# Kernel optimization log

Hardware: AMD Instinct MI355X
Metric: run time of the kernel (lower is better)

Reference implementation:

```python
import jax, jax.numpy as jnp
import numpy as np

PERCENTAGE = 0.26
BN_EPS = 1e-5


def _conv1x1(x, w, b):
    # x: (B,C,H,W), w: (O,C), b: (O,)
    return jnp.einsum('bchw,oc->bohw', x, w) + b[None, :, None, None]


def _bn_train(x, gamma, beta):
    # BatchNorm2d in training mode: biased variance over (B,H,W) per channel
    mean = x.mean(axis=(0, 2, 3), keepdims=True)
    var = jnp.mean((x - mean) ** 2, axis=(0, 2, 3), keepdims=True)
    xhat = (x - mean) * jax.lax.rsqrt(var + BN_EPS)
    return xhat * gamma[None, :, None, None] + beta[None, :, None, None]


def _band_mask(w, max_w):
    # The two mask-construction loops in the torch code reduce to |i-j| < max_w
    idx = jnp.arange(w)
    return jnp.abs(idx[:, None] - idx[None, :]) < max_w  # (w, w) bool


def setup_inputs() -> dict:
    key = jax.random.key(0)
    ks = jax.random.split(key, 16)
    B, C, H, W = 2, 256, 64, 512
    s = 0.02  # weight scale to keep attention logits in a sane range
    return {
        'x1': jax.random.normal(ks[0], (B, C, H, W), jnp.float32),
        'x2': jax.random.normal(ks[1], (B, C, H, W), jnp.float32),
        'Qw': jax.random.normal(ks[2], (C, C), jnp.float32) * s,
        'Qb': jax.random.normal(ks[3], (C,), jnp.float32) * s,
        'Kw': jax.random.normal(ks[4], (C, C), jnp.float32) * s,
        'Kb': jax.random.normal(ks[5], (C,), jnp.float32) * s,
        'Vw': jax.random.normal(ks[6], (C, C), jnp.float32) * s,
        'Vb': jax.random.normal(ks[7], (C,), jnp.float32) * s,
        'Vg': jax.random.normal(ks[8], (C,), jnp.float32),
        'Vbeta': jax.random.normal(ks[9], (C,), jnp.float32),
        'Ww': jax.random.normal(ks[10], (C, C), jnp.float32) * s,
        'Wb': jax.random.normal(ks[11], (C,), jnp.float32) * s,
        'Wg': jax.random.normal(ks[12], (C,), jnp.float32),
        'Wbeta': jax.random.normal(ks[13], (C,), jnp.float32),
    }


def reference(x1, x2, Qw, Qb, Kw, Kb, Vw, Vb, Vg, Vbeta, Ww, Wb, Wg, Wbeta):
    b, c, h, w = x1.shape
    max_w = int(w * PERCENTAGE)
    mask = _band_mask(w, max_w)  # (w, w), broadcasts over (b*h) rows
    neg_inf = jnp.float32(-jnp.inf)

    def rows(x):  # (B,C,H,W) -> (B*H, W, C)
        return x.transpose(0, 2, 3, 1).reshape(b * h, w, c)

    q1 = rows(_conv1x1(x1, Qw, Qb))
    q2 = rows(_conv1x1(x2, Qw, Qb))
    k1 = rows(_conv1x1(x1, Kw, Kb))  # (B*H, W, C); contract over C below
    k2 = rows(_conv1x1(x2, Kw, Kb))
    v1 = rows(_bn_train(_conv1x1(x1, Vw, Vb), Vg, Vbeta))
    v2 = rows(_bn_train(_conv1x1(x2, Vw, Vb), Vg, Vbeta))

    def attend(q, k, v):
        scores = jnp.einsum('nqc,nkc->nqk', q, k)  # (B*H, W, W)
        scores = jnp.where(mask[None], scores, neg_inf)
        p = jax.nn.softmax(scores, axis=-1)
        return jnp.einsum('nqk,nkc->nqc', p, v)

    def cols(y):  # (B*H, W, C) -> (B,C,H,W)
        return y.reshape(b, h, w, c).transpose(0, 3, 1, 2)

    y1 = cols(attend(q1, k2, v2))
    y2 = cols(attend(q2, k1, v1))
    z1 = _bn_train(_conv1x1(y1, Ww, Wb), Wg, Wbeta) + x1
    z2 = _bn_train(_conv1x1(y2, Ww, Wb), Wg, Wbeta) + x2
    return (z1, z2)
```

## Files before the change

### kernel.cpp

```cpp
#include <hip/hip_runtime.h>

typedef unsigned short u16;
typedef short bfrag __attribute__((ext_vector_type(8)));
typedef float ffrag __attribute__((ext_vector_type(4)));
typedef u16 u16x4 __attribute__((ext_vector_type(4)));
typedef float f4 __attribute__((ext_vector_type(4)));

#define MFMA16(a,b,c) __builtin_amdgcn_mfma_f32_16x16x32_bf16((a),(b),(c),0,0,0)

#define WAITV(N) do { asm volatile("s_waitcnt vmcnt(" #N ")" ::: "memory"); \
                      __builtin_amdgcn_sched_barrier(0); } while(0)
#define RBAR()   do { __builtin_amdgcn_s_barrier(); \
                      __builtin_amdgcn_sched_barrier(0); } while(0)


__device__ __forceinline__ u16 f2bf(float f){
  union { float f; unsigned int i; } cv; cv.f = f;
  unsigned int x = cv.i;
  return (u16)((x + 0x7fffu + ((x >> 16) & 1u)) >> 16);
}
__device__ __forceinline__ float bf2f(u16 u){
  union { unsigned int i; float f; } cv;
  cv.i = ((unsigned int)u) << 16;
  return cv.f;
}
__device__ __forceinline__ unsigned cvtpk(float lo, float hi){
  unsigned r; asm("v_cvt_pk_bf16_f32 %0, %1, %2" : "=v"(r) : "v"(lo), "v"(hi)); return r;
}
__device__ __forceinline__ bfrag ldb(const u16* p){
  bfrag v; __builtin_memcpy(&v, p, 16); return v;
}
__device__ __forceinline__ void gload_lds16(const u16* g, u16* l){
  __builtin_amdgcn_global_load_lds(
      (const __attribute__((address_space(1))) unsigned int*)g,
      (__attribute__((address_space(3))) unsigned int*)l, 16, 0, 0);
}

__global__ __launch_bounds__(256) void k_wcvt(const float* __restrict__ qw, const float* __restrict__ kw,
                                              const float* __restrict__ vw, const float* __restrict__ ww,
                                              u16* __restrict__ out){
  int t = blockIdx.x*256 + threadIdx.x;
  out[t]        = f2bf(qw[t]);
  out[t+65536]  = f2bf(kw[t]);
  out[t+131072] = f2bf(vw[t]);
  out[t+196608] = f2bf(ww[t]);
}

__global__ __launch_bounds__(256) void k_xpose(const float* __restrict__ x1, const float* __restrict__ x2,
                                               u16* __restrict__ xr1, u16* __restrict__ xr2){
  const float* x = blockIdx.z ? x2 : x1;
  u16* xr = blockIdx.z ? xr2 : xr1;
  __shared__ float T[64][65];
  int t = threadIdx.x;
  int p0 = blockIdx.x*64, c0 = blockIdx.y*64;
  int b = p0 >> 15, q0 = p0 & 32767;
  #pragma unroll
  for (int it=0; it<4; ++it){
    int cc = it*16 + (t>>4);
    int pi = (t&15)*4;
    ffrag v; __builtin_memcpy(&v, x + ((size_t)(b*256 + c0 + cc))*32768 + q0 + pi, 16);
    T[cc][pi+0]=v[0]; T[cc][pi+1]=v[1]; T[cc][pi+2]=v[2]; T[cc][pi+3]=v[3];
  }
  __syncthreads();
  int pi = t>>2, cj0 = (t&3)*16;
  u16 tmp[16];
  #pragma unroll
  for (int j=0;j<16;++j) tmp[j] = f2bf(T[cj0+j][pi]);
  __builtin_memcpy(xr + (size_t)(p0+pi)*256 + c0 + cj0, tmp, 32);
}

template<int NI>
__device__ __forceinline__ void stageT(const u16* __restrict__ src, int row0, int k0,
                                       u16* lds, int wid, int l){
  #pragma unroll
  for (int rr=0; rr<NI; ++rr){
    int off = rr*4096 + wid*1024 + l*16;
    int row = off>>7, inb = off&127;
    int srcb = inb ^ ((row&7)<<4);
    gload_lds16(src + (size_t)(row0+row)*256 + k0 + (srcb>>1),
                lds + ((rr*4096 + wid*1024)>>1));
  }
}

__global__ __launch_bounds__(256, 3) void k_qkv(const u16* __restrict__ xr1, const u16* __restrict__ xr2,
    const u16* __restrict__ wb,
    const float* __restrict__ qb, const float* __restrict__ kb, const float* __restrict__ vb,
    u16* __restrict__ Q1, u16* __restrict__ K1, u16* __restrict__ V1,
    u16* __restrict__ Q2, u16* __restrict__ K2, u16* __restrict__ V2){
  __shared__ __align__(16) u16 As[2][8192];
  __shared__ __align__(16) u16 Bs[2][4096];
  int id = blockIdx.x;
  int xcd = id & 7, j = id >> 3;
  int pl = j/24, v = j - pl*24;
  int ptile = xcd*64 + pl;
  int ot = v & 3, r = v >> 2;
  int wgt = r >> 1, s = r & 1;
  const u16* A = s ? xr2 : xr1;
  const u16* W = wb + wgt*65536;
  const float* bias = (wgt==0)? qb : (wgt==1)? kb : vb;

  int t = threadIdx.x, wid = t>>6, l = t&63, lr = l&15, lg = l>>4;
  int p0 = ptile*128, o0 = ot*64;
  int wr = wid*32;
  int swz = (lr&7)<<4;

  stageT<4>(A, p0, 0,  As[0], wid, l);
  stageT<2>(W, o0, 0,  Bs[0], wid, l);
  stageT<4>(A, p0, 64, As[1], wid, l);
  stageT<2>(W, o0, 64, Bs[1], wid, l);

  const ffrag fz = {0.f,0.f,0.f,0.f};
  ffrag acc[2][4];
  #pragma unroll
  for (int i=0;i<2;++i){ acc[i][0]=fz; acc[i][1]=fz; acc[i][2]=fz; acc[i][3]=fz; }

  #pragma unroll
  for (int ks=0; ks<4; ++ks){
    if (ks < 3) { WAITV(6); } else { WAITV(0); }
    RBAR();
    const u16* as = As[ks&1];
    const u16* bs = Bs[ks&1];
    #pragma unroll
    for (int kc=0; kc<2; ++kc){
      int colb = (kc*64 + lg*16) ^ swz;
      bfrag af[2], bf[4];
      #pragma unroll
      for (int mt=0; mt<2; ++mt)
        af[mt] = ldb(as + (((wr + mt*16 + lr)*128 + colb)>>1));
      #pragma unroll
      for (int nt=0; nt<4; ++nt)
        bf[nt] = ldb(bs + (((nt*16 + lr)*128 + colb)>>1));
      if (wgt != 2){
        #pragma unroll
        for (int mt=0; mt<2; ++mt)
          #pragma unroll
          for (int nt=0; nt<4; ++nt)
            acc[mt][nt] = MFMA16(bf[nt], af[mt], acc[mt][nt]);
      } else {
        #pragma unroll
        for (int mt=0; mt<2; ++mt)
          #pragma unroll
          for (int nt=0; nt<4; ++nt)
            acc[mt][nt] = MFMA16(af[mt], bf[nt], acc[mt][nt]);
      }
    }
    RBAR();
    if (ks < 2){
      stageT<4>(A, p0, (ks+2)*64, As[ks&1], wid, l);
      stageT<2>(W, o0, (ks+2)*64, Bs[ks&1], wid, l);
    }
  }

  if (wgt != 2){
    u16* op = (wgt==0) ? (s ? Q2 : Q1) : (s ? K2 : K1);
    #pragma unroll
    for (int nt=0; nt<4; ++nt){
      int ob = o0 + nt*16 + lg*4;
      ffrag bv = *reinterpret_cast<const ffrag*>(bias + ob);
      #pragma unroll
      for (int mt=0; mt<2; ++mt){
        int p = p0 + wr + mt*16 + lr;
        u16x4 vv;
        #pragma unroll
        for (int rr=0;rr<4;++rr) vv[rr] = f2bf(acc[mt][nt][rr] + bv[rr]);
        *reinterpret_cast<u16x4*>(op + (size_t)p*256 + ob) = vv;
      }
    }
  } else {
    u16* Vt = s ? V2 : V1;
    #pragma unroll
    for (int nt=0; nt<4; ++nt){
      int oo = o0 + nt*16 + lr;
      float bsc = bias[oo];
      #pragma unroll
      for (int mt=0; mt<2; ++mt){
        int pr = p0 + wr + mt*16 + lg*4;
        int n = pr >> 9, w0 = pr & 511;
        u16x4 vv;
        #pragma unroll
        for (int rr=0;rr<4;++rr) vv[rr] = f2bf(acc[mt][nt][rr] + bsc);
        *reinterpret_cast<u16x4*>(Vt + ((size_t)(n*256 + oo))*512 + w0) = vv;
      }
    }
  }
}

__global__ __launch_bounds__(256, 2) void k_conv1(const u16* __restrict__ in1, const u16* __restrict__ in2,
    const u16* __restrict__ wp, const float* __restrict__ bias,
    u16* __restrict__ o1, u16* __restrict__ o2,
    float* __restrict__ psum, float* __restrict__ psq){
  __shared__ __align__(16) u16 As[2][8192];
  __shared__ __align__(16) u16 Bs[2][8192];
  int id = blockIdx.x;
  int xcd = id & 7, j = id >> 3;
  int pl = j>>2, v = j&3;
  int ptile = xcd*64 + pl;
  int ot = v & 1, s = v >> 1;
  const u16* A = s ? in2 : in1;
  u16* out = s ? o2 : o1;

  int t = threadIdx.x, wid = t>>6, l = t&63, lr = l&15, lg = l>>4;
  int p0 = ptile*128, o0 = ot*128;
  int wr = (wid>>1)*64, wc = (wid&1)*64;
  int swz = (lr&7)<<4;

  stageT<4>(A, p0, 0,  As[0], wid, l);
  stageT<4>(wp, o0, 0, Bs[0], wid, l);
  stageT<4>(A, p0, 64, As[1], wid, l);
  stageT<4>(wp, o0, 64,Bs[1], wid, l);

  const ffrag fz = {0.f,0.f,0.f,0.f};
  ffrag acc[4][4];
  #pragma unroll
  for (int i=0;i<4;++i){ acc[i][0]=fz; acc[i][1]=fz; acc[i][2]=fz; acc[i][3]=fz; }

  #pragma unroll
  for (int ks=0; ks<4; ++ks){
    if (ks < 3) { WAITV(8); } else { WAITV(0); }
    RBAR();
    const u16* as = As[ks&1];
    const u16* bs = Bs[ks&1];
    #pragma unroll
    for (int kc=0; kc<2; ++kc){
      int colb = (kc*64 + lg*16) ^ swz;
      bfrag af[4], bfm[4];
      #pragma unroll
      for (int mt=0; mt<4; ++mt)
        af[mt] = ldb(as + (((wr + mt*16 + lr)*128 + colb)>>1));
      #pragma unroll
      for (int nt=0; nt<4; ++nt)
        bfm[nt] = ldb(bs + (((wc + nt*16 + lr)*128 + colb)>>1));
      #pragma unroll
      for (int mt=0; mt<4; ++mt)
        #pragma unroll
        for (int nt=0; nt<4; ++nt)
          acc[mt][nt] = MFMA16(af[mt], bfm[nt], acc[mt][nt]);
    }
    RBAR();
    if (ks < 2){
      stageT<4>(A, p0, (ks+2)*64, As[ks&1], wid, l);
      stageT<4>(wp, o0, (ks+2)*64, Bs[ks&1], wid, l);
    }
  }

  float pv[4], qv[4];
  #pragma unroll
  for (int nt=0; nt<4; ++nt){ pv[nt]=0.f; qv[nt]=0.f; }
  #pragma unroll
  for (int nt=0; nt<4; ++nt){
    int oo = o0 + wc + nt*16 + lr;
    float bsc = bias[oo];
    #pragma unroll
    for (int mt=0; mt<4; ++mt){
      int pr = p0 + wr + mt*16 + lg*4;
      #pragma unroll
      for (int rr=0;rr<4;++rr){
        float val = acc[mt][nt][rr] + bsc;
        out[(size_t)(pr + rr)*256 + oo] = f2bf(val);
        pv[nt] += val; qv[nt] += val*val;
      }
    }
  }
  #pragma unroll
  for (int nt=0; nt<4; ++nt){
    float sv = pv[nt], sq = qv[nt];
    sv += __shfl_xor(sv,16,64); sv += __shfl_xor(sv,32,64);
    sq += __shfl_xor(sq,16,64); sq += __shfl_xor(sq,32,64);
    if (lg==0){
      int oo = o0 + wc + nt*16 + lr;
      int idx = ((s*256 + oo)<<10) + (ptile<<1) + (wr>>6);
      psum[idx] = sv; psq[idx] = sq;
    }
  }
}

__global__ __launch_bounds__(256) void k_vstat1(const u16* __restrict__ V1, const u16* __restrict__ V2,
                                                float* __restrict__ ps, float* __restrict__ pq){
  int s = blockIdx.z;
  const u16* Vt = s ? V2 : V1;
  int c = blockIdx.x, ch = blockIdx.y, t = threadIdx.x;
  const u16* base = Vt + ((size_t)((ch*16 + (t>>4))*256 + c))*512 + (t&15)*32;
  float sm=0.f, sq=0.f;
  #pragma unroll
  for (int j=0;j<4;++j){
    bfrag v = ldb(base + j*8);
    #pragma unroll
    for (int e=0;e<8;++e){ float f = bf2f((u16)v[e]); sm+=f; sq+=f*f; }
  }
  __shared__ float rs[256], rq[256];
  rs[t]=sm; rq[t]=sq; __syncthreads();
  for (int st=128; st>0; st>>=1){ if (t<st){ rs[t]+=rs[t+st]; rq[t]+=rq[t+st]; } __syncthreads(); }
  if (t==0){ ps[s*2048 + c*8+ch]=rs[0]; pq[s*2048 + c*8+ch]=rq[0]; }
}
__global__ __launch_bounds__(256) void k_vstat2(const float* __restrict__ ps, const float* __restrict__ pq,
                                                const float* __restrict__ g, const float* __restrict__ be,
                                                float* __restrict__ aVall, float* __restrict__ bVall){
  int s = blockIdx.x, c = threadIdx.x;
  float sm=0.f, sq=0.f;
  #pragma unroll
  for (int ch=0; ch<8; ++ch){ sm += ps[s*2048 + c*8+ch]; sq += pq[s*2048 + c*8+ch]; }
  float mean = sm*(1.f/65536.f);
  float var  = sq*(1.f/65536.f) - mean*mean;
  float aa = g[c]*rsqrtf(var + 1e-5f);
  aVall[s*256+c]=aa; bVall[s*256+c]=be[c]-aa*mean;
}

__device__ __forceinline__ void stageK(const u16* Kn, u16* kb, int kt, int wid, int l){
  #pragma unroll
  for (int c2=0; c2<2; ++c2){
    int off = wid*2048 + c2*1024 + l*16;
    int row = off>>9, inb = off&511;
    int src = inb ^ ((row&7)<<4);
    gload_lds16(Kn + (size_t)(kt*16+row)*256 + (src>>1), kb + wid*1024 + c2*512);
  }
}
__device__ __forceinline__ void stageV(const u16* Vn, u16* vb, int k0, int wid, int l){
  #pragma unroll
  for (int c4=0; c4<4; ++c4){
    int off = wid*4096 + c4*1024 + l*16;
    int crow = off>>6, slot = (off>>4)&3;
    int kk = slot ^ ((crow>>1)&3);
    gload_lds16(Vn + (size_t)crow*512 + k0 + (kk<<3), vb + ((wid*4096 + c4*1024)>>1));
  }
}

__global__ __launch_bounds__(256, 2) void k_attn(
    const u16* __restrict__ Q1, const u16* __restrict__ K2, const u16* __restrict__ V2,
    const u16* __restrict__ Q2, const u16* __restrict__ K1, const u16* __restrict__ V1,
    const float* __restrict__ aVall, const float* __restrict__ bVall,
    u16* __restrict__ O1, u16* __restrict__ O2){
  __shared__ __align__(16) u16 KP[2][8192];
  __shared__ __align__(16) u16 VBs[2][8192];
  int t = threadIdx.x, wid = t>>6, l = t&63, lr = l&15, lg = l>>4;
  int id = blockIdx.x;
  int s = id >> 10;
  int r0 = id & 1023;
  int xcd = r0 & 7, s5 = r0 >> 3;
  int qb = s5 & 7, n = (xcd<<4) | (s5>>3);
  const u16* Q = s ? Q2 : Q1;
  const u16* K = s ? K1 : K2;
  const u16* V = s ? V1 : V2;
  const float* aV = aVall + (s ? 0 : 256);
  const float* bV = bVall + (s ? 0 : 256);
  u16* O = s ? O2 : O1;

  int q0 = qb*64, q0w = q0 + wid*16;
  int lo = q0 - 132; if (lo < 0) lo = 0;
  int hi = q0 + 195; if (hi > 511) hi = 511;
  int KTLO = (lo>>4) & ~1;
  int KTHI = (hi>>4) | 1;
  int nsteps = (KTHI - KTLO + 2) >> 1;

  const u16* Kn = K + (size_t)n*131072;
  const u16* Vn = V + (size_t)n*131072;

  bfrag qa[8];
  const u16* Qrow = Q + ((size_t)(n*512 + q0w + lr))*256 + lg*8;
  #pragma unroll
  for (int ks=0; ks<8; ++ks) qa[ks] = ldb(Qrow + ks*32);
  WAITV(0);

  stageK(Kn, KP[0],        KTLO+0, wid, l);
  stageK(Kn, KP[0]+4096,   KTLO+1, wid, l);
  stageV(Vn, VBs[0],       KTLO*16 + 0,  wid, l);
  stageK(Kn, KP[1],        KTLO+2, wid, l);
  stageK(Kn, KP[1]+4096,   KTLO+3, wid, l);
  stageV(Vn, VBs[1],       KTLO*16 + 32, wid, l);

  const ffrag fz = {0.f,0.f,0.f,0.f};
  ffrag o[16];
  #pragma unroll
  for (int i=0;i<16;++i) o[i] = fz;
  float lsum = 0.f;
  int q = q0w + lr;
  int s0l = lr + (lg&1)*32;
  bool hi2 = (lg & 2) != 0;
  int vswz = (lg ^ ((lr>>1)&3))<<3;

  #pragma unroll
  for (int sp=0; sp<12; ++sp){
    if (sp < nsteps){
      if (sp < nsteps-1) { WAITV(8); } else { WAITV(0); }
      RBAR();
      const u16* kp = KP[sp&1];
      const u16* vb = VBs[sp&1];

      ffrag sA = fz, sB = fz;
      #pragma unroll
      for (int ks=0; ks<8; ++ks){
        int boff = (ks*64 + lg*16) ^ ((lr&7)<<4);
        bfrag kfA = ldb(kp + ((lr*512 + boff)>>1));
        bfrag kfB = ldb(kp + 4096 + ((lr*512 + boff)>>1));
        sA = MFMA16(kfA, qa[ks], sA);
        sB = MFMA16(kfB, qa[ks], sB);
      }

      int baseA = q + 132 - ((KTLO + 2*sp)*16 + lg*4);
      #pragma unroll
      for (int r=0;r<4;++r){
        bool vA = (unsigned)(baseA - r)      < 265u;
        bool vB = (unsigned)(baseA - r - 16) < 265u;
        float eA = vA ? __expf(sA[r]) : 0.f;
        float eB = vB ? __expf(sB[r]) : 0.f;
        sA[r] = eA; sB[r] = eB; lsum += eA + eB;
      }

      unsigned pk0A = cvtpk(sA[0], sA[1]);
      unsigned pk1A = cvtpk(sA[2], sA[3]);
      unsigned pk0B = cvtpk(sB[0], sB[1]);
      unsigned pk1B = cvtpk(sB[2], sB[3]);
      unsigned a0 = (unsigned)__shfl((int)pk0A, s0l,    64);
      unsigned a1 = (unsigned)__shfl((int)pk1A, s0l,    64);
      unsigned a2 = (unsigned)__shfl((int)pk0A, s0l+16, 64);
      unsigned a3 = (unsigned)__shfl((int)pk1A, s0l+16, 64);
      unsigned b0 = (unsigned)__shfl((int)pk0B, s0l,    64);
      unsigned b1 = (unsigned)__shfl((int)pk1B, s0l,    64);
      unsigned b2 = (unsigned)__shfl((int)pk0B, s0l+16, 64);
      unsigned b3 = (unsigned)__shfl((int)pk1B, s0l+16, 64);
      unsigned pu[4];
      pu[0] = hi2 ? b0 : a0;  pu[1] = hi2 ? b1 : a1;
      pu[2] = hi2 ? b2 : a2;  pu[3] = hi2 ? b3 : a3;
      bfrag pa; __builtin_memcpy(&pa, pu, 16);

      #pragma unroll
      for (int ct=0; ct<16; ++ct){
        bfrag vf = ldb(vb + (ct*16 + lr)*32 + vswz);
        o[ct] = MFMA16(pa, vf, o[ct]);
      }
      RBAR();
      if (sp+2 < nsteps){
        stageK(Kn, KP[sp&1],      KTLO + 2*sp + 4, wid, l);
        stageK(Kn, KP[sp&1]+4096, KTLO + 2*sp + 5, wid, l);
        stageV(Vn, VBs[sp&1],     KTLO*16 + (sp+2)*32, wid, l);
      }
    }
  }

  lsum += __shfl_xor(lsum, 16, 64);
  lsum += __shfl_xor(lsum, 32, 64);
  float rinv = 1.f / lsum;
  float linv[4];
  #pragma unroll
  for (int r=0;r<4;++r) linv[r] = __shfl(rinv, (lg<<2)+r, 64);
  #pragma unroll
  for (int ct=0; ct<16; ++ct){
    int c = ct*16 + lr;
    float av = aV[c], bv = bV[c];
    #pragma unroll
    for (int r=0;r<4;++r)
      O[((size_t)(n*512 + q0w + lg*4 + r))*256 + c] = f2bf(av*(o[ct][r]*linv[r]) + bv);
  }
}

__global__ __launch_bounds__(256) void k_ustat2(const float* __restrict__ psum, const float* __restrict__ psq,
                                                const float* __restrict__ g, const float* __restrict__ be,
                                                float* __restrict__ aWall, float* __restrict__ bWall){
  int c = blockIdx.x, s = blockIdx.y, t = threadIdx.x;
  const float* ps = psum + (((size_t)s*256 + c)<<10);
  const float* pq = psq  + (((size_t)s*256 + c)<<10);
  float sm = ps[t] + ps[t+256] + ps[t+512] + ps[t+768];
  float sq = pq[t] + pq[t+256] + pq[t+512] + pq[t+768];
  __shared__ float rs[256], rq[256];
  rs[t]=sm; rq[t]=sq; __syncthreads();
  for (int st=128; st>0; st>>=1){ if (t<st){ rs[t]+=rs[t+st]; rq[t]+=rq[t+st]; } __syncthreads(); }
  if (t==0){
    float mean = rs[0]*(1.f/65536.f);
    float var  = rq[0]*(1.f/65536.f) - mean*mean;
    float aa = g[c]*rsqrtf(var + 1e-5f);
    aWall[s*256+c]=aa; bWall[s*256+c]=be[c]-aa*mean;
  }
}

__global__ __launch_bounds__(256) void k_final(const u16* __restrict__ u1, const u16* __restrict__ u2,
                                               const u16* __restrict__ xr1, const u16* __restrict__ xr2,
                                               const float* __restrict__ aWall, const float* __restrict__ bWall,
                                               float* __restrict__ z){
  int s = blockIdx.z;
  const u16* u  = s ? u2 : u1;
  const u16* xr = s ? xr2 : xr1;
  const float* aW = aWall + s*256;
  const float* bW = bWall + s*256;
  float* zb = z + (size_t)s*16777216;
  __shared__ u16 Tu[64][66], Tx[64][66];
  int t = threadIdx.x;
  int p0 = blockIdx.x*64, c0 = blockIdx.y*64;
  int b = p0>>15, q0 = p0&32767;
  #pragma unroll
  for (int it=0; it<4; ++it){
    int pi = it*16 + (t>>4);
    int cj = (t&15)*4;
    u16x4 vu; __builtin_memcpy(&vu, u  + (size_t)(p0+pi)*256 + c0 + cj, 8);
    u16x4 vx; __builtin_memcpy(&vx, xr + (size_t)(p0+pi)*256 + c0 + cj, 8);
    *reinterpret_cast<u16x4*>(&Tu[pi][cj]) = vu;
    *reinterpret_cast<u16x4*>(&Tx[pi][cj]) = vx;
  }
  __syncthreads();
  int qi4 = (t&15)*4;
  #pragma unroll
  for (int it=0; it<4; ++it){
    int cc = it*16 + (t>>4);
    float a = aW[c0+cc], bw = bW[c0+cc];
    f4 vz;
    #pragma unroll
    for (int j=0;j<4;++j)
      vz[j] = a*bf2f(Tu[qi4+j][cc]) + bw + bf2f(Tx[qi4+j][cc]);
    *reinterpret_cast<f4*>(zb + ((size_t)(b*256 + c0 + cc))*32768 + q0 + qi4) = vz;
  }
}

extern "C" void kernel_launch(void* const* d_in, const int* in_sizes, int n_in,
                              void* d_out, int out_size, void* d_ws, size_t ws_size,
                              hipStream_t stream) {
  const float* x1  = (const float*)d_in[0];
  const float* x2  = (const float*)d_in[1];
  const float* Qw  = (const float*)d_in[2];
  const float* Qb  = (const float*)d_in[3];
  const float* Kw  = (const float*)d_in[4];
  const float* Kb  = (const float*)d_in[5];
  const float* Vw  = (const float*)d_in[6];
  const float* Vb  = (const float*)d_in[7];
  const float* Vg  = (const float*)d_in[8];
  const float* Vbe = (const float*)d_in[9];
  const float* Ww  = (const float*)d_in[10];
  const float* Wb  = (const float*)d_in[11];
  const float* Wg  = (const float*)d_in[12];
  const float* Wbe = (const float*)d_in[13];

  char* ws = (char*)d_ws;
  const size_t S = 33554432;
  u16* xr1 = (u16*)(ws + 0*S);
  u16* xr2 = (u16*)(ws + 1*S);
  u16* Q1  = (u16*)(ws + 2*S);
  u16* K1  = (u16*)(ws + 3*S);
  u16* Q2  = (u16*)(ws + 4*S);
  u16* K2  = (u16*)(ws + 5*S);
  u16* wb  = (u16*)(ws + 6*S);
  float* vec = (float*)(ws + 6*S + 524288);
  float* aVall = vec;
  float* bVall = vec + 512;
  float* aWall = vec + 1024;
  float* bWall = vec + 1536;
  float* vps   = vec + 2048;
  float* vpq   = vps + 4096;

  char* douts = (char*)d_out;
  u16* Vt1 = (u16*)douts;
  u16* Vt2 = (u16*)(douts + S);
  u16* O1  = (u16*)(douts + 2*S);
  u16* O2  = (u16*)(douts + 3*S);
  float* upsum = (float*)douts;
  float* upsq  = upsum + 524288;
  u16* u1 = Q1;  u16* u2 = K1;
  float* z = (float*)d_out;

  dim3 gt(1024, 4, 2);
  dim3 gv(256, 8, 2);
  dim3 gu2(256, 2);

  k_wcvt<<<256, 256, 0, stream>>>(Qw, Kw, Vw, Ww, wb);
  k_xpose<<<gt, 256, 0, stream>>>(x1, x2, xr1, xr2);
  k_qkv<<<12288, 256, 0, stream>>>(xr1, xr2, wb, Qb, Kb, Vb, Q1, K1, Vt1, Q2, K2, Vt2);
  k_vstat1<<<gv, 256, 0, stream>>>(Vt1, Vt2, vps, vpq);
  k_vstat2<<<2, 256, 0, stream>>>(vps, vpq, Vg, Vbe, aVall, bVall);
  k_attn<<<2048, 256, 0, stream>>>(Q1, K2, Vt2, Q2, K1, Vt1, aVall, bVall, O1, O2);
  k_conv1<<<2048, 256, 0, stream>>>(O1, O2, wb + 196608, Wb, u1, u2, upsum, upsq);
  k_ustat2<<<gu2, 256, 0, stream>>>(upsum, upsq, Wg, Wbe, aWall, bWall);
  k_final<<<gt, 256, 0, stream>>>(u1, u2, xr1, xr2, aWall, bWall, z);
}
```

Measured before the change: 339.2 us.

## Fold Q and K projections into one merged weight and per-key bias term

Rewrites the attention scores as (x Qw^T Kw) x^T plus a per-key term, since the query bias and all key-bias contributions are constant along the softmax row except Qb·Kw·x_k. A merged weight Wq^T Wk is precomputed, the QKV GEMM now produces only XM and V, and attention reads the raw bf16 x as keys plus a precomputed per-key scalar c2 added before exp. This cuts a third of the projection GEMM work and the K writes, at the cost of extra small kernels, an extra bf16 rounding of the merged weight, and per-step c2 loads in the attention loop.

```diff
diff --git a/kernel.cpp b/kernel.cpp
--- a/kernel.cpp
+++ b/kernel.cpp
@@ -46,6 +46,47 @@
   out[t+196608] = f2bf(ww[t]);
 }
 
+__global__ __launch_bounds__(256) void k_g(const float* __restrict__ Qb, const u16* __restrict__ wb,
+                                           float* __restrict__ g){
+  int t = threadIdx.x;
+  float sm = 0.f;
+  #pragma unroll 8
+  for (int o=0;o<256;++o) sm += Qb[o]*bf2f(wb[65536 + o*256 + t]);
+  g[t] = sm;
+}
+
+__global__ __launch_bounds__(256) void k_mg(const u16* __restrict__ wb, u16* __restrict__ wm){
+  int c = blockIdx.x, t = threadIdx.x;
+  float sm = 0.f;
+  #pragma unroll 8
+  for (int o=0;o<256;++o) sm += bf2f(wb[o*256 + c]) * bf2f(wb[65536 + o*256 + t]);
+  wm[t*256 + c] = f2bf(sm);
+}
+
+__global__ __launch_bounds__(256) void k_c2(const u16* __restrict__ xr1, const u16* __restrict__ xr2,
+                                            const float* __restrict__ g, float* __restrict__ c2){
+  __shared__ float gs[256];
+  int t = threadIdx.x;
+  gs[t] = g[t];
+  __syncthreads();
+  int s = blockIdx.y;
+  const u16* xr = s ? xr2 : xr1;
+  float* out = c2 + s*65536;
+  int l = t & 63, w = t >> 6;
+  int half = l >> 5, cl = l & 31;
+  for (int it=0; it<16; ++it){
+    int row = blockIdx.x*128 + w*32 + it*2 + half;
+    bfrag v = ldb(xr + (size_t)row*256 + cl*8);
+    float sm = 0.f;
+    #pragma unroll
+    for (int e=0;e<8;++e) sm += bf2f((u16)v[e]) * gs[cl*8 + e];
+    sm += __shfl_xor(sm,1,64);  sm += __shfl_xor(sm,2,64);
+    sm += __shfl_xor(sm,4,64);  sm += __shfl_xor(sm,8,64);
+    sm += __shfl_xor(sm,16,64);
+    if (cl==0) out[row] = sm;
+  }
+}
+
 __global__ __launch_bounds__(256) void k_xpose(const float* __restrict__ x1, const float* __restrict__ x2,
                                                u16* __restrict__ xr1, u16* __restrict__ xr2){
   const float* x = blockIdx.z ? x2 : x1;
@@ -83,21 +124,20 @@
 }
 
 __global__ __launch_bounds__(256, 3) void k_qkv(const u16* __restrict__ xr1, const u16* __restrict__ xr2,
-    const u16* __restrict__ wb,
-    const float* __restrict__ qb, const float* __restrict__ kb, const float* __restrict__ vb,
-    u16* __restrict__ Q1, u16* __restrict__ K1, u16* __restrict__ V1,
-    u16* __restrict__ Q2, u16* __restrict__ K2, u16* __restrict__ V2){
+    const u16* __restrict__ wb, const u16* __restrict__ wm,
+    const float* __restrict__ vb,
+    u16* __restrict__ XM1, u16* __restrict__ V1,
+    u16* __restrict__ XM2, u16* __restrict__ V2){
   __shared__ __align__(16) u16 As[2][8192];
   __shared__ __align__(16) u16 Bs[2][4096];
   int id = blockIdx.x;
   int xcd = id & 7, j = id >> 3;
-  int pl = j/24, v = j - pl*24;
+  int pl = j >> 4, v = j & 15;
   int ptile = xcd*64 + pl;
   int ot = v & 3, r = v >> 2;
-  int wgt = r >> 1, s = r & 1;
+  int wgtV = r >> 1, s = r & 1;
   const u16* A = s ? xr2 : xr1;
-  const u16* W = wb + wgt*65536;
-  const float* bias = (wgt==0)? qb : (wgt==1)? kb : vb;
+  const u16* W = wgtV ? (wb + 131072) : wm;
 
   int t = threadIdx.x, wid = t>>6, l = t&63, lr = l&15, lg = l>>4;
   int p0 = ptile*128, o0 = ot*64;
@@ -130,7 +170,7 @@
       #pragma unroll
       for (int nt=0; nt<4; ++nt)
         bf[nt] = ldb(bs + (((nt*16 + lr)*128 + colb)>>1));
-      if (wgt != 2){
+      if (!wgtV){
         #pragma unroll
         for (int mt=0; mt<2; ++mt)
           #pragma unroll
@@ -151,18 +191,17 @@
     }
   }
 
-  if (wgt != 2){
-    u16* op = (wgt==0) ? (s ? Q2 : Q1) : (s ? K2 : K1);
+  if (!wgtV){
+    u16* op = s ? XM2 : XM1;
     #pragma unroll
     for (int nt=0; nt<4; ++nt){
       int ob = o0 + nt*16 + lg*4;
-      ffrag bv = *reinterpret_cast<const ffrag*>(bias + ob);
       #pragma unroll
       for (int mt=0; mt<2; ++mt){
         int p = p0 + wr + mt*16 + lr;
         u16x4 vv;
         #pragma unroll
-        for (int rr=0;rr<4;++rr) vv[rr] = f2bf(acc[mt][nt][rr] + bv[rr]);
+        for (int rr=0;rr<4;++rr) vv[rr] = f2bf(acc[mt][nt][rr]);
         *reinterpret_cast<u16x4*>(op + (size_t)p*256 + ob) = vv;
       }
     }
@@ -171,7 +210,7 @@
     #pragma unroll
     for (int nt=0; nt<4; ++nt){
       int oo = o0 + nt*16 + lr;
-      float bsc = bias[oo];
+      float bsc = vb[oo];
       #pragma unroll
       for (int mt=0; mt<2; ++mt){
         int pr = p0 + wr + mt*16 + lg*4;
@@ -325,9 +364,10 @@
 }
 
 __global__ __launch_bounds__(256, 2) void k_attn(
-    const u16* __restrict__ Q1, const u16* __restrict__ K2, const u16* __restrict__ V2,
-    const u16* __restrict__ Q2, const u16* __restrict__ K1, const u16* __restrict__ V1,
+    const u16* __restrict__ XM1, const u16* __restrict__ xr2, const u16* __restrict__ V2,
+    const u16* __restrict__ XM2, const u16* __restrict__ xr1, const u16* __restrict__ V1,
     const float* __restrict__ aVall, const float* __restrict__ bVall,
+    const float* __restrict__ c2all,
     u16* __restrict__ O1, u16* __restrict__ O2){
   __shared__ __align__(16) u16 KP[2][8192];
   __shared__ __align__(16) u16 VBs[2][8192];
@@ -337,11 +377,12 @@
   int r0 = id & 1023;
   int xcd = r0 & 7, s5 = r0 >> 3;
   int qb = s5 & 7, n = (xcd<<4) | (s5>>3);
-  const u16* Q = s ? Q2 : Q1;
-  const u16* K = s ? K1 : K2;
+  const u16* Q = s ? XM2 : XM1;
+  const u16* K = s ? xr1 : xr2;
   const u16* V = s ? V1 : V2;
   const float* aV = aVall + (s ? 0 : 256);
   const float* bV = bVall + (s ? 0 : 256);
+  const float* c2k = c2all + ((s^1)<<16) + n*512;
   u16* O = s ? O2 : O1;
 
   int q0 = qb*64, q0w = q0 + wid*16;
@@ -358,6 +399,13 @@
   const u16* Qrow = Q + ((size_t)(n*512 + q0w + lr))*256 + lg*8;
   #pragma unroll
   for (int ks=0; ks<8; ++ks) qa[ks] = ldb(Qrow + ks*32);
+  f4 c2A, c2B, c2An, c2Bn;
+  {
+    int colb0 = KTLO*16 + lg*4;
+    c2A = *reinterpret_cast<const f4*>(c2k + colb0);
+    c2B = *reinterpret_cast<const f4*>(c2k + colb0 + 16);
+    c2An = c2A; c2Bn = c2B;
+  }
   WAITV(0);
 
   stageK(Kn, KP[0],        KTLO+0, wid, l);
@@ -380,7 +428,9 @@
   #pragma unroll
   for (int sp=0; sp<12; ++sp){
     if (sp < nsteps){
-      if (sp < nsteps-1) { WAITV(8); } else { WAITV(0); }
+      if (sp == 0) { WAITV(8); }
+      else if (sp < nsteps-1) { WAITV(10); }
+      else { WAITV(0); }
       RBAR();
       const u16* kp = KP[sp&1];
       const u16* vb = VBs[sp&1];
@@ -400,8 +450,8 @@
       for (int r=0;r<4;++r){
         bool vA = (unsigned)(baseA - r)      < 265u;
         bool vB = (unsigned)(baseA - r - 16) < 265u;
-        float eA = vA ? __expf(sA[r]) : 0.f;
-        float eB = vB ? __expf(sB[r]) : 0.f;
+        float eA = vA ? __expf(sA[r] + c2A[r]) : 0.f;
+        float eB = vB ? __expf(sB[r] + c2B[r]) : 0.f;
         sA[r] = eA; sB[r] = eB; lsum += eA + eB;
       }
 
@@ -427,12 +477,19 @@
         bfrag vf = ldb(vb + (ct*16 + lr)*32 + vswz);
         o[ct] = MFMA16(pa, vf, o[ct]);
       }
+
+      if (sp+1 < nsteps){
+        int colbN = (KTLO + 2*(sp+1))*16 + lg*4;
+        c2An = *reinterpret_cast<const f4*>(c2k + colbN);
+        c2Bn = *reinterpret_cast<const f4*>(c2k + colbN + 16);
+      }
       RBAR();
       if (sp+2 < nsteps){
         stageK(Kn, KP[sp&1],      KTLO + 2*sp + 4, wid, l);
         stageK(Kn, KP[sp&1]+4096, KTLO + 2*sp + 5, wid, l);
         stageV(Vn, VBs[sp&1],     KTLO*16 + (sp+2)*32, wid, l);
       }
+      c2A = c2An; c2B = c2Bn;
     }
   }
 
@@ -525,15 +582,16 @@
   const float* Wb  = (const float*)d_in[11];
   const float* Wg  = (const float*)d_in[12];
   const float* Wbe = (const float*)d_in[13];
+  (void)Kb;
 
   char* ws = (char*)d_ws;
   const size_t S = 33554432;
   u16* xr1 = (u16*)(ws + 0*S);
   u16* xr2 = (u16*)(ws + 1*S);
-  u16* Q1  = (u16*)(ws + 2*S);
-  u16* K1  = (u16*)(ws + 3*S);
-  u16* Q2  = (u16*)(ws + 4*S);
-  u16* K2  = (u16*)(ws + 5*S);
+  u16* XM1 = (u16*)(ws + 2*S);
+  u16* u1  = (u16*)(ws + 3*S);
+  u16* XM2 = (u16*)(ws + 4*S);
+  u16* u2  = (u16*)(ws + 5*S);
   u16* wb  = (u16*)(ws + 6*S);
   float* vec = (float*)(ws + 6*S + 524288);
   float* aVall = vec;
@@ -541,7 +599,10 @@
   float* aWall = vec + 1024;
   float* bWall = vec + 1536;
   float* vps   = vec + 2048;
-  float* vpq   = vps + 4096;
+  float* vpq   = vec + 6144;
+  u16*   wm    = (u16*)(vec + 10240);
+  float* g     = vec + 43008;
+  float* c2all = vec + 43264;
 
   char* douts = (char*)d_out;
   u16* Vt1 = (u16*)douts;
@@ -550,19 +611,22 @@
   u16* O2  = (u16*)(douts + 3*S);
   float* upsum = (float*)douts;
   float* upsq  = upsum + 524288;
-  u16* u1 = Q1;  u16* u2 = K1;
   float* z = (float*)d_out;
 
   dim3 gt(1024, 4, 2);
+  dim3 gc2(512, 2);
   dim3 gv(256, 8, 2);
   dim3 gu2(256, 2);
 
   k_wcvt<<<256, 256, 0, stream>>>(Qw, Kw, Vw, Ww, wb);
+  k_g<<<1, 256, 0, stream>>>(Qb, wb, g);
+  k_mg<<<256, 256, 0, stream>>>(wb, wm);
   k_xpose<<<gt, 256, 0, stream>>>(x1, x2, xr1, xr2);
-  k_qkv<<<12288, 256, 0, stream>>>(xr1, xr2, wb, Qb, Kb, Vb, Q1, K1, Vt1, Q2, K2, Vt2);
+  k_c2<<<gc2, 256, 0, stream>>>(xr1, xr2, g, c2all);
+  k_qkv<<<8192, 256, 0, stream>>>(xr1, xr2, wb, wm, Vb, XM1, Vt1, XM2, Vt2);
   k_vstat1<<<gv, 256, 0, stream>>>(Vt1, Vt2, vps, vpq);
   k_vstat2<<<2, 256, 0, stream>>>(vps, vpq, Vg, Vbe, aVall, bVall);
-  k_attn<<<2048, 256, 0, stream>>>(Q1, K2, Vt2, Q2, K1, Vt1, aVall, bVall, O1, O2);
+  k_attn<<<2048, 256, 0, stream>>>(XM1, xr2, Vt2, XM2, xr1, Vt1, aVall, bVall, c2all, O1, O2);
   k_conv1<<<2048, 256, 0, stream>>>(O1, O2, wb + 196608, Wb, u1, u2, upsum, upsq);
   k_ustat2<<<gu2, 256, 0, stream>>>(upsum, upsq, Wg, Wbe, aWall, bWall);
   k_final<<<gt, 256, 0, stream>>>(u1, u2, xr1, xr2, aWall, bWall, z);
```

Measured after the change: 347.8 us. +2.5%, slower.
